# Optimization experiments

Hardware: AMD Instinct MI355X
Metric: run time of the kernel (lower is better)

Reference implementation:

```python
import jax, jax.numpy as jnp
import numpy as np

HEADS = 8
DIM_HEAD = 32
SCALE = DIM_HEAD ** -0.5


def setup_inputs() -> dict:
    key = jax.random.key(0)
    k1, k2, k3 = jax.random.split(key, 3)
    B, H, W, C = 16, 64, 64, 256
    hidden = HEADS * DIM_HEAD  # 256
    x = jax.random.normal(k1, (B, H, W, C), dtype=jnp.float32)
    # 1x1 convs with no bias == dense matmuls over channel dim (glorot-ish scale)
    w_qkv = jax.random.normal(k2, (C, 3 * hidden), dtype=jnp.float32) * (1.0 / np.sqrt(C))
    w_out = jax.random.normal(k3, (hidden, C), dtype=jnp.float32) * (1.0 / np.sqrt(hidden))
    return {"x": x, "w_qkv": w_qkv, "w_out": w_out}


def reference(x, w_qkv, w_out):
    B, H, W, C = x.shape
    n = H * W
    # to_qkv: 1x1 conv, no bias
    qkv = jnp.einsum('bhwc,cf->bhwf', x, w_qkv)  # [B,H,W,3*hidden]
    q, k, v = jnp.split(qkv, 3, axis=-1)

    def to_heads(t):
        # 'b x y (h c) -> b h c (x y)'
        t = t.reshape(B, n, HEADS, DIM_HEAD)
        return jnp.transpose(t, (0, 2, 3, 1))  # [B, heads, dim_head, n]

    q, k, v = to_heads(q), to_heads(k), to_heads(v)
    q = jax.nn.softmax(q, axis=-2) * SCALE      # softmax over feature dim d
    k = jax.nn.softmax(k, axis=-1)              # softmax over spatial dim n
    context = jnp.einsum('bhdn,bhen->bhde', k, v)   # [B, heads, d, e]
    out = jnp.einsum('bhde,bhdn->bhen', context, q)  # [B, heads, e, n]
    # 'b h c (x y) -> b x y (h c)'
    out = jnp.transpose(out, (0, 3, 1, 2)).reshape(B, H, W, HEADS * DIM_HEAD)
    # to_out: 1x1 conv, no bias
    return jnp.einsum('bhwf,fc->bhwc', out, w_out)
```

## Files before the change

kernel.cpp:

```cpp
#include <hip/hip_runtime.h>

using short8 = __attribute__((ext_vector_type(8))) short;
using f32x4  = __attribute__((ext_vector_type(4))) float;

#define SCALE_Q 0.17677669529663687f
#define NCHUNK 16

__device__ __forceinline__ unsigned short f2bf(float f) {
  unsigned u = __float_as_uint(f);
  return (unsigned short)((u + 0x7FFFu + ((u >> 16) & 1u)) >> 16);
}
__device__ __forceinline__ float bf2f(unsigned h) { return __uint_as_float(h << 16); }

__device__ __forceinline__ void bf8_to_f(uint4 r, float* o) {
  o[0] = bf2f(r.x & 0xffffu); o[1] = bf2f(r.x >> 16);
  o[2] = bf2f(r.y & 0xffffu); o[3] = bf2f(r.y >> 16);
  o[4] = bf2f(r.z & 0xffffu); o[5] = bf2f(r.z >> 16);
  o[6] = bf2f(r.w & 0xffffu); o[7] = bf2f(r.w >> 16);
}

__device__ __forceinline__ void gl_lds16(const unsigned short* g, unsigned short* l) {
  __builtin_amdgcn_global_load_lds(
      (const __attribute__((address_space(1))) void*)g,
      (__attribute__((address_space(3))) void*)l, 16, 0, 0);
}

__global__ __launch_bounds__(256) void prep_kernel(
    const float* __restrict__ x, const float* __restrict__ wqkv, const float* __restrict__ wout,
    unsigned short* __restrict__ xb, unsigned short* __restrict__ wqkvT,
    unsigned short* __restrict__ woutT) {
  const int blk = blockIdx.x;
  if (blk < 16384) {
    const size_t i = ((size_t)blk * 256 + threadIdx.x) * 4;
    const float4 v = *(const float4*)(x + i);
    *(ushort4*)(xb + i) = make_ushort4(f2bf(v.x), f2bf(v.y), f2bf(v.z), f2bf(v.w));
  } else if (blk < 16384 + 768) {
    const int n = blk - 16384, k = threadIdx.x;
    wqkvT[n * 256 + k] = f2bf(wqkv[(size_t)k * 768 + n]);
  } else {
    const int c = blk - 16384 - 768, f = threadIdx.x;
    woutT[c * 256 + f] = f2bf(wout[(size_t)f * 256 + c]);
  }
}

template <typename OutT, bool QKV>
__global__ __launch_bounds__(256, 2) void gemm_bregs(
    const unsigned short* __restrict__ A, const unsigned short* __restrict__ BT,
    OutT* __restrict__ D, unsigned short* __restrict__ QS,
    int NSTRIP, int TPB,
    size_t strideA, size_t strideB, size_t strideD) {
  __shared__ unsigned short As[128 * 256];
  const int xcd = blockIdx.x & 7, idx = blockIdx.x >> 3;
  const int strip = idx % NSTRIP;
  const int mg = xcd + (idx / NSTRIP) * 8;
  const int z = blockIdx.z;
  const int tid = threadIdx.x, lane = tid & 63, wid = tid >> 6;
  const int fr = lane & 15, hi = lane >> 4;

  const unsigned short* Bb = BT + (size_t)z * strideB + (size_t)strip * 64 * 256;
  short8 breg[4][8];
#pragma unroll
  for (int nj = 0; nj < 4; ++nj)
#pragma unroll
    for (int kk = 0; kk < 8; ++kk)
      breg[nj][kk] = *(const short8*)(Bb + (size_t)(nj * 16 + fr) * 256 + kk * 32 + hi * 8);

  const int srow = tid >> 5;
  const int schunk = (tid & 31) ^ srow;
  const size_t sgoff = (size_t)srow * 256 + schunk * 8;
  unsigned short* lds_w = As + wid * 512;

  for (int t = 0; t < TPB; ++t) {
    const size_t row0 = (size_t)(mg * TPB + t) * 128;
    const unsigned short* Ag = A + (size_t)z * strideA + row0 * 256 + sgoff;
#pragma unroll
    for (int r = 0; r < 16; ++r) gl_lds16(Ag + r * 2048, lds_w + r * 2048);
    __syncthreads();

    f32x4 acc[2][4] = {};
#pragma unroll
    for (int kk = 0; kk < 8; ++kk) {
      short8 af[2];
#pragma unroll
      for (int mi = 0; mi < 2; ++mi) {
        const int row = wid * 32 + mi * 16 + fr;
        const int ch = (kk * 4 + hi) ^ (fr & 7);
        af[mi] = *(const short8*)&As[row * 256 + ch * 8];
      }
#pragma unroll
      for (int mi = 0; mi < 2; ++mi)
#pragma unroll
        for (int nj = 0; nj < 4; ++nj)
          acc[mi][nj] = __builtin_amdgcn_mfma_f32_16x16x32_bf16(af[mi], breg[nj][kk], acc[mi][nj], 0, 0, 0);
    }

    if (QKV && strip < 4) {
#pragma unroll
      for (int mi = 0; mi < 2; ++mi)
#pragma unroll
        for (int p = 0; p < 2; ++p)
#pragma unroll
          for (int r = 0; r < 4; ++r) {
            const float v0 = acc[mi][2 * p][r], v1 = acc[mi][2 * p + 1][r];
            float mx = fmaxf(v0, v1);
#pragma unroll
            for (int xm = 1; xm < 16; xm <<= 1) mx = fmaxf(mx, __shfl_xor(mx, xm, 64));
            const float e0 = __expf(v0 - mx), e1 = __expf(v1 - mx);
            float s = e0 + e1;
#pragma unroll
            for (int xm = 1; xm < 16; xm <<= 1) s += __shfl_xor(s, xm, 64);
            const float inv = SCALE_Q / s;
            const size_t row = row0 + wid * 32 + mi * 16 + hi * 4 + r;
            QS[row * 256 + strip * 64 + p * 32 + fr]      = f2bf(e0 * inv);
            QS[row * 256 + strip * 64 + p * 32 + 16 + fr] = f2bf(e1 * inv);
          }
    } else {
      const int c0 = QKV ? (strip * 64 - 256) : (strip * 64);
      const int ncols = QKV ? 512 : 256;
      OutT* Dz = D + (size_t)z * strideD;
#pragma unroll
      for (int mi = 0; mi < 2; ++mi)
#pragma unroll
        for (int nj = 0; nj < 4; ++nj) {
          const int col = c0 + nj * 16 + fr;
#pragma unroll
          for (int r = 0; r < 4; ++r) {
            const size_t row = row0 + wid * 32 + mi * 16 + hi * 4 + r;
            const float v = acc[mi][nj][r];
            if constexpr (sizeof(OutT) == 2) Dz[row * ncols + col] = (OutT)f2bf(v);
            else                             Dz[row * ncols + col] = v;
          }
        }
    }
    __syncthreads();
  }
}

__global__ __launch_bounds__(256) void ctx_part_kernel(const unsigned short* __restrict__ kv,
                                                       float* __restrict__ part,
                                                       float* __restrict__ spart) {
  const int blk = blockIdx.x;
  const int bh = blk >> 4, chunk = blk & 15;
  const int b = bh >> 3, h = bh & 7;
  const int tid = threadIdx.x, d = tid & 31, g = tid >> 5;
  const unsigned short* kbase =
      kv + (size_t)b * 4096 * 512 + h * 32 + (size_t)chunk * 256 * 512;
  const unsigned short* vbase = kbase + 256;

  __shared__ float ek[64][36], vv[64][36];
  float a0 = 0.f, a1 = 0.f, a2 = 0.f, a3 = 0.f, ssum = 0.f;
  const int e0 = g * 4;
  const int sn = tid >> 2, sc = (tid & 3) * 8;
  const unsigned short* kp0 = kbase + (size_t)sn * 512 + sc;
  const unsigned short* vp0 = vbase + (size_t)sn * 512 + sc;
  uint4 kr = *(const uint4*)kp0;
  uint4 vr = *(const uint4*)vp0;
  for (int n0 = 0; n0 < 256; n0 += 64) {
    float kf[8], vf[8];
    bf8_to_f(kr, kf); bf8_to_f(vr, vf);
    uint4 krn = kr, vrn = vr;
    if (n0 + 64 < 256) {
      krn = *(const uint4*)(kp0 + (size_t)(n0 + 64) * 512);
      vrn = *(const uint4*)(vp0 + (size_t)(n0 + 64) * 512);
    }
#pragma unroll
    for (int j = 0; j < 8; ++j) { ek[sn][sc + j] = __expf(kf[j]); vv[sn][sc + j] = vf[j]; }
    __syncthreads();
#pragma unroll 8
    for (int i = 0; i < 64; ++i) {
      const float kd = ek[i][d];
      const float4 v4 = *(const float4*)&vv[i][e0];
      ssum += kd;
      a0 += kd * v4.x; a1 += kd * v4.y; a2 += kd * v4.z; a3 += kd * v4.w;
    }
    __syncthreads();
    kr = krn; vr = vrn;
  }
  float* pp = part + ((size_t)chunk * 128 + bh) * 1024 + d * 32 + e0;
  pp[0] = a0; pp[1] = a1; pp[2] = a2; pp[3] = a3;
  if (g == 0) spart[((size_t)chunk * 128 + bh) * 32 + d] = ssum;
}

__global__ __launch_bounds__(256) void ctx_combine_kernel(const float* __restrict__ part,
                                                          const float* __restrict__ spart,
                                                          float* __restrict__ ctx) {
  const int bh = blockIdx.x, tid = threadIdx.x;
  __shared__ float sinv[32];
  if (tid < 32) {
    float s = 0.f;
#pragma unroll
    for (int c = 0; c < NCHUNK; ++c) s += spart[((size_t)c * 128 + bh) * 32 + tid];
    sinv[tid] = 1.0f / s;
  }
  __syncthreads();
  float4 acc = make_float4(0.f, 0.f, 0.f, 0.f);
#pragma unroll
  for (int c = 0; c < NCHUNK; ++c) {
    const float4 p = *(const float4*)(part + ((size_t)c * 128 + bh) * 1024 + tid * 4);
    acc.x += p.x; acc.y += p.y; acc.z += p.z; acc.w += p.w;
  }
  const float si = sinv[tid >> 3];
  float4* cp = (float4*)(ctx + (size_t)bh * 1024 + tid * 4);
  *cp = make_float4(acc.x * si, acc.y * si, acc.z * si, acc.w * si);
}

__global__ __launch_bounds__(256) void w2_kernel(const float* __restrict__ ctx,
                                                 const unsigned short* __restrict__ woutT,
                                                 unsigned short* __restrict__ W2T) {
  const int b = blockIdx.x >> 4, cg = blockIdx.x & 15;
  const int tid = threadIdx.x;
  __shared__ float cs[8 * 32 * 32];
  {
    const float4* src = (const float4*)(ctx + (size_t)b * 8192);
    float4* dst = (float4*)cs;
#pragma unroll
    for (int i = 0; i < 8; ++i) dst[tid + i * 256] = src[tid + i * 256];
  }
  __syncthreads();
  const int c = cg * 16 + (tid >> 4), chunk = tid & 15;
  const int h = chunk >> 1, d0 = (chunk & 1) * 16;
  float wf[32];
  {
    const uint4* wp = (const uint4*)(woutT + (size_t)c * 256 + h * 32);
    bf8_to_f(wp[0], wf + 0); bf8_to_f(wp[1], wf + 8);
    bf8_to_f(wp[2], wf + 16); bf8_to_f(wp[3], wf + 24);
  }
  unsigned short o[16];
#pragma unroll
  for (int dd = 0; dd < 16; ++dd) {
    const float* cp = cs + h * 1024 + (d0 + dd) * 32;
    float acc = 0.f;
#pragma unroll
    for (int e = 0; e < 32; ++e) acc += cp[e] * wf[e];
    o[dd] = f2bf(acc);
  }
  uint4* op = (uint4*)(W2T + ((size_t)b * 256 + c) * 256 + chunk * 16);
  op[0] = make_uint4((unsigned)o[0] | ((unsigned)o[1] << 16), (unsigned)o[2] | ((unsigned)o[3] << 16),
                     (unsigned)o[4] | ((unsigned)o[5] << 16), (unsigned)o[6] | ((unsigned)o[7] << 16));
  op[1] = make_uint4((unsigned)o[8] | ((unsigned)o[9] << 16), (unsigned)o[10] | ((unsigned)o[11] << 16),
                     (unsigned)o[12] | ((unsigned)o[13] << 16), (unsigned)o[14] | ((unsigned)o[15] << 16));
}

extern "C" void kernel_launch(void* const* d_in, const int* in_sizes, int n_in,
                              void* d_out, int out_size, void* d_ws, size_t ws_size,
                              hipStream_t stream) {
  const float* x     = (const float*)d_in[0];
  const float* wqkv  = (const float*)d_in[1];
  const float* wout  = (const float*)d_in[2];
  float* out = (float*)d_out;

  char* ws = (char*)d_ws;
  unsigned short* xb    = (unsigned short*)(ws);
  unsigned short* wqkvT = (unsigned short*)(ws + 33554432);
  unsigned short* woutT = (unsigned short*)(ws + 33947648);
  unsigned short* kv    = (unsigned short*)(ws + 34078720);
  float*          ctx   = (float*)        (ws + 101187584);
  unsigned short* qs    = (unsigned short*)(ws + 101711872);
  float*          part  = (float*)(ws);
  float*          spart = (float*)(ws + 8388608);
  unsigned short* W2T   = (unsigned short*)(ws + 12582912);

  prep_kernel<<<16384 + 768 + 256, 256, 0, stream>>>(x, wqkv, wout, xb, wqkvT, woutT);
  gemm_bregs<unsigned short, true><<<1536, 256, 0, stream>>>(
      xb, wqkvT, kv, qs, 12, 4, 0, 0, 0);
  ctx_part_kernel<<<2048, 256, 0, stream>>>(kv, part, spart);
  ctx_combine_kernel<<<128, 256, 0, stream>>>(part, spart, ctx);
  w2_kernel<<<256, 256, 0, stream>>>(ctx, woutT, W2T);
  gemm_bregs<float, false><<<dim3(32, 1, 16), 256, 0, stream>>>(
      qs, W2T, out, nullptr, 4, 4,
      (size_t)4096 * 256, (size_t)256 * 256, (size_t)4096 * 256);
}
```

Baseline: 177.4 us.

## Per-wave LDS staging with A-tile prefetch and transposed MFMA operands in GEMMs

Rewrites the GEMM kernel so each wave loads its own 32-row A slice into a private LDS region. The next tile is prefetched with global_load_lds while the MFMAs on the current one run, which removes the block-wide __syncthreads. MFMA operands are swapped so each lane holds four consecutive output columns, allowing vectorized ushort4/float4 stores and a cheaper softmax reduction needing only two cross-lane shuffles. Tile counts become template parameters. The risks are register pressure from keeping whole A fragments in registers and hand-placed waitcnt/sched_barrier ordering.

```diff
diff --git a/kernel.cpp b/kernel.cpp
--- a/kernel.cpp
+++ b/kernel.cpp
@@ -43,96 +43,123 @@
   }
 }
 
-template <typename OutT, bool QKV>
-__global__ __launch_bounds__(256, 2) void gemm_bregs(
+template <typename OutT, bool QKV, int NSTRIP, int TPB>
+__global__ __launch_bounds__(256, 2) void gemm_ws(
     const unsigned short* __restrict__ A, const unsigned short* __restrict__ BT,
     OutT* __restrict__ D, unsigned short* __restrict__ QS,
-    int NSTRIP, int TPB,
     size_t strideA, size_t strideB, size_t strideD) {
-  __shared__ unsigned short As[128 * 256];
+  __shared__ unsigned short lds[4 * 8192];
   const int xcd = blockIdx.x & 7, idx = blockIdx.x >> 3;
   const int strip = idx % NSTRIP;
   const int mg = xcd + (idx / NSTRIP) * 8;
   const int z = blockIdx.z;
-  const int tid = threadIdx.x, lane = tid & 63, wid = tid >> 6;
+  const int lane = threadIdx.x & 63, wid = threadIdx.x >> 6;
   const int fr = lane & 15, hi = lane >> 4;
 
-  const unsigned short* Bb = BT + (size_t)z * strideB + (size_t)strip * 64 * 256;
+  const unsigned short* Az = A + (size_t)z * strideA;
+  unsigned short* wlds = lds + wid * 8192;
+
+  {
+    const size_t row0 = ((size_t)mg * TPB) * 128 + wid * 32;
+    const unsigned short* Ap = Az + (row0 + fr) * 256 + hi * 8;
+#pragma unroll
+    for (int mi = 0; mi < 2; ++mi)
+#pragma unroll
+      for (int kk = 0; kk < 8; ++kk)
+        gl_lds16(Ap + ((size_t)mi * 16) * 256 + kk * 32, wlds + (mi * 8 + kk) * 512);
+  }
   short8 breg[4][8];
-#pragma unroll
-  for (int nj = 0; nj < 4; ++nj)
+  {
+    const unsigned short* Bp = BT + (size_t)z * strideB + ((size_t)strip * 64 + fr) * 256 + hi * 8;
+#pragma unroll
+    for (int nj = 0; nj < 4; ++nj)
+#pragma unroll
+      for (int kk = 0; kk < 8; ++kk)
+        breg[nj][kk] = *(const short8*)(Bp + (size_t)nj * 16 * 256 + kk * 32);
+  }
+
+  for (int t = 0; t < TPB; ++t) {
+    const size_t row0 = ((size_t)mg * TPB + t) * 128 + wid * 32;
+    asm volatile("s_waitcnt vmcnt(0)" ::: "memory");
+    __builtin_amdgcn_sched_barrier(0);
+    short8 cur[2][8];
+#pragma unroll
+    for (int mi = 0; mi < 2; ++mi)
+#pragma unroll
+      for (int kk = 0; kk < 8; ++kk)
+        cur[mi][kk] = *(const short8*)(wlds + (mi * 8 + kk) * 512 + lane * 8);
+    asm volatile("s_waitcnt lgkmcnt(0)" ::: "memory");
+    __builtin_amdgcn_sched_barrier(0);
+    if (t + 1 < TPB) {
+      const unsigned short* Ap = Az + (row0 + 128 + fr) * 256 + hi * 8;
+#pragma unroll
+      for (int mi = 0; mi < 2; ++mi)
+#pragma unroll
+        for (int kk = 0; kk < 8; ++kk)
+          gl_lds16(Ap + ((size_t)mi * 16) * 256 + kk * 32, wlds + (mi * 8 + kk) * 512);
+    }
+    __builtin_amdgcn_sched_barrier(0);
+
+    f32x4 acc[2][4] = {};
 #pragma unroll
     for (int kk = 0; kk < 8; ++kk)
-      breg[nj][kk] = *(const short8*)(Bb + (size_t)(nj * 16 + fr) * 256 + kk * 32 + hi * 8);
-
-  const int srow = tid >> 5;
-  const int schunk = (tid & 31) ^ srow;
-  const size_t sgoff = (size_t)srow * 256 + schunk * 8;
-  unsigned short* lds_w = As + wid * 512;
-
-  for (int t = 0; t < TPB; ++t) {
-    const size_t row0 = (size_t)(mg * TPB + t) * 128;
-    const unsigned short* Ag = A + (size_t)z * strideA + row0 * 256 + sgoff;
-#pragma unroll
-    for (int r = 0; r < 16; ++r) gl_lds16(Ag + r * 2048, lds_w + r * 2048);
-    __syncthreads();
-
-    f32x4 acc[2][4] = {};
-#pragma unroll
-    for (int kk = 0; kk < 8; ++kk) {
-      short8 af[2];
+#pragma unroll
+      for (int mi = 0; mi < 2; ++mi)
+#pragma unroll
+        for (int nj = 0; nj < 4; ++nj)
+          acc[mi][nj] = __builtin_amdgcn_mfma_f32_16x16x32_bf16(breg[nj][kk], cur[mi][kk], acc[mi][nj], 0, 0, 0);
+
+    if (QKV && strip < 4) {
 #pragma unroll
       for (int mi = 0; mi < 2; ++mi) {
-        const int row = wid * 32 + mi * 16 + fr;
-        const int ch = (kk * 4 + hi) ^ (fr & 7);
-        af[mi] = *(const short8*)&As[row * 256 + ch * 8];
+        const size_t row = row0 + mi * 16 + fr;
+#pragma unroll
+        for (int p = 0; p < 2; ++p) {
+          const f32x4 v0 = acc[mi][2 * p], v1 = acc[mi][2 * p + 1];
+          float mx = fmaxf(fmaxf(fmaxf(v0[0], v0[1]), fmaxf(v0[2], v0[3])),
+                           fmaxf(fmaxf(v1[0], v1[1]), fmaxf(v1[2], v1[3])));
+          mx = fmaxf(mx, __shfl_xor(mx, 16, 64));
+          mx = fmaxf(mx, __shfl_xor(mx, 32, 64));
+          float e0[4], e1[4], s = 0.f;
+#pragma unroll
+          for (int r = 0; r < 4; ++r) {
+            e0[r] = __expf(v0[r] - mx); e1[r] = __expf(v1[r] - mx);
+            s += e0[r] + e1[r];
+          }
+          s += __shfl_xor(s, 16, 64);
+          s += __shfl_xor(s, 32, 64);
+          const float inv = SCALE_Q / s;
+          unsigned short* qp = QS + row * 256 + (strip * 2 + p) * 32 + hi * 4;
+          *(ushort4*)(qp)      = make_ushort4(f2bf(e0[0]*inv), f2bf(e0[1]*inv), f2bf(e0[2]*inv), f2bf(e0[3]*inv));
+          *(ushort4*)(qp + 16) = make_ushort4(f2bf(e1[0]*inv), f2bf(e1[1]*inv), f2bf(e1[2]*inv), f2bf(e1[3]*inv));
+        }
       }
-#pragma unroll
-      for (int mi = 0; mi < 2; ++mi)
-#pragma unroll
-        for (int nj = 0; nj < 4; ++nj)
-          acc[mi][nj] = __builtin_amdgcn_mfma_f32_16x16x32_bf16(af[mi], breg[nj][kk], acc[mi][nj], 0, 0, 0);
-    }
-
-    if (QKV && strip < 4) {
-#pragma unroll
-      for (int mi = 0; mi < 2; ++mi)
-#pragma unroll
-        for (int p = 0; p < 2; ++p)
-#pragma unroll
-          for (int r = 0; r < 4; ++r) {
-            const float v0 = acc[mi][2 * p][r], v1 = acc[mi][2 * p + 1][r];
-            float mx = fmaxf(v0, v1);
-#pragma unroll
-            for (int xm = 1; xm < 16; xm <<= 1) mx = fmaxf(mx, __shfl_xor(mx, xm, 64));
-            const float e0 = __expf(v0 - mx), e1 = __expf(v1 - mx);
-            float s = e0 + e1;
-#pragma unroll
-            for (int xm = 1; xm < 16; xm <<= 1) s += __shfl_xor(s, xm, 64);
-            const float inv = SCALE_Q / s;
-            const size_t row = row0 + wid * 32 + mi * 16 + hi * 4 + r;
-            QS[row * 256 + strip * 64 + p * 32 + fr]      = f2bf(e0 * inv);
-            QS[row * 256 + strip * 64 + p * 32 + 16 + fr] = f2bf(e1 * inv);
-          }
+    } else if (QKV) {
+#pragma unroll
+      for (int mi = 0; mi < 2; ++mi) {
+        const size_t row = row0 + mi * 16 + fr;
+#pragma unroll
+        for (int nj = 0; nj < 4; ++nj) {
+          const f32x4 v = acc[mi][nj];
+          unsigned short* kp = QS , *dp = (unsigned short*)D;
+          dp += row * 512 + (size_t)(strip - 4) * 64 + nj * 16 + hi * 4;
+          *(ushort4*)dp = make_ushort4(f2bf(v[0]), f2bf(v[1]), f2bf(v[2]), f2bf(v[3]));
+          (void)kp;
+        }
+      }
     } else {
-      const int c0 = QKV ? (strip * 64 - 256) : (strip * 64);
-      const int ncols = QKV ? 512 : 256;
       OutT* Dz = D + (size_t)z * strideD;
 #pragma unroll
-      for (int mi = 0; mi < 2; ++mi)
+      for (int mi = 0; mi < 2; ++mi) {
+        const size_t row = row0 + mi * 16 + fr;
 #pragma unroll
         for (int nj = 0; nj < 4; ++nj) {
-          const int col = c0 + nj * 16 + fr;
-#pragma unroll
-          for (int r = 0; r < 4; ++r) {
-            const size_t row = row0 + wid * 32 + mi * 16 + hi * 4 + r;
-            const float v = acc[mi][nj][r];
-            if constexpr (sizeof(OutT) == 2) Dz[row * ncols + col] = (OutT)f2bf(v);
-            else                             Dz[row * ncols + col] = v;
-          }
+          const f32x4 v = acc[mi][nj];
+          float* dp = (float*)(Dz + row * 256 + strip * 64 + nj * 16 + hi * 4);
+          *(float4*)dp = make_float4(v[0], v[1], v[2], v[3]);
         }
-    }
-    __syncthreads();
+      }
+    }
   }
 }
 
@@ -261,12 +288,11 @@
   unsigned short* W2T   = (unsigned short*)(ws + 12582912);
 
   prep_kernel<<<16384 + 768 + 256, 256, 0, stream>>>(x, wqkv, wout, xb, wqkvT, woutT);
-  gemm_bregs<unsigned short, true><<<1536, 256, 0, stream>>>(
-      xb, wqkvT, kv, qs, 12, 4, 0, 0, 0);
+  gemm_ws<unsigned short, true, 12, 4><<<1536, 256, 0, stream>>>(
+      xb, wqkvT, kv, qs, 0, 0, 0);
   ctx_part_kernel<<<2048, 256, 0, stream>>>(kv, part, spart);
   ctx_combine_kernel<<<128, 256, 0, stream>>>(part, spart, ctx);
   w2_kernel<<<256, 256, 0, stream>>>(ctx, woutT, W2T);
-  gemm_bregs<float, false><<<dim3(32, 1, 16), 256, 0, stream>>>(
-      qs, W2T, out, nullptr, 4, 4,
-      (size_t)4096 * 256, (size_t)256 * 256, (size_t)4096 * 256);
-}
+  gemm_ws<float, false, 4, 4><<<dim3(32, 1, 16), 256, 0, stream>>>(
+      qs, W2T, out, nullptr, (size_t)4096 * 256, (size_t)256 * 256, (size_t)4096 * 256);
+}
```

Result: slower. 190.4 us (+7.3%).
